# Kernel optimization log

Measured on AMD Instinct MI355X. Metric: run time of the kernel, lower is better.

Reference implementation:

```python
import jax, jax.numpy as jnp
import numpy as np
from math import pi

H = 1024        # hidden_size
CAP = 32        # capacity (even -> CAP//2 even+odd rotation pairs)
EH = H // 2         # even_hidden_size = 512
OH = (H - 1) // 2   # odd_hidden_size  = 511
PAIRS = CAP // 2    # 16

# fixed permutations (hidden_size even branch of the original module)
_PE = np.arange(H).reshape(-1, 2)[:, ::-1].reshape(-1)                       # swap (0,1),(2,3),...
_inner = np.arange(1, 2 * OH + 1).reshape(-1, 2)[:, ::-1].reshape(-1)
_PO = np.concatenate([[0], _inner, [2 * OH + 1]])                            # fix ends, swap interior pairs


def cm(x, y):
    """complex multiply; real/imag stacked in last dim."""
    xr, xi = x[..., 0], x[..., 1]
    yr, yi = y[..., 0], y[..., 1]
    return jnp.stack([xr * yr - xi * yi, xr * yi + xi * yr], -1)


def _ilv(a, b):
    """interleave two [n] vectors -> [2n]."""
    return jnp.stack([a, b], 1).reshape(-1)


def setup_inputs() -> dict:
    key = jax.random.key(0)
    ks = jax.random.split(key, 6)
    u = lambda k, shape: jax.random.uniform(k, shape, jnp.float32) * (2 * pi) - pi
    return {
        "x": jax.random.normal(ks[0], (4096, H, 2), jnp.float32),
        "omega": u(ks[1], (H,)),
        "even_theta": u(ks[2], (PAIRS, EH)),
        "odd_theta": u(ks[3], (PAIRS, OH)),
        "even_phi": u(ks[4], (PAIRS, EH)),
        "odd_phi": u(ks[5], (PAIRS, OH)),
    }


def reference(x, omega, even_theta, odd_theta, even_phi, odd_phi):
    PE = jnp.asarray(_PE)
    PO = jnp.asarray(_PO)

    def step(xc, p):
        et, ep, ot, op = p
        # ---- even rotation (note: original code swaps cos_phi/sin_phi in the
        # call to _v_diag/_v_off_diag; replicated faithfully here) ----
        ct, st, cp, sp = jnp.cos(et), jnp.sin(et), jnp.cos(ep), jnp.sin(ep)
        z = jnp.zeros_like(ct)
        vd = jnp.stack([_ilv(sp * ct, ct), _ilv(cp * ct, z)], -1)          # [H,2]
        vo = jnp.stack([_ilv(-sp * st, st), _ilv(-cp * st, z)], -1)        # [H,2]
        xc = cm(xc, vd) + cm(xc[:, PE, :], vo)
        # ---- odd rotation (ends padded with identity) ----
        ct, st, cp, sp = jnp.cos(ot), jnp.sin(ot), jnp.cos(op), jnp.sin(op)
        z = jnp.zeros_like(ct)
        one = jnp.ones((1,), xc.dtype)
        zero = jnp.zeros((1,), xc.dtype)
        vd_re = jnp.concatenate([one, _ilv(sp * ct, ct), one])
        vd_im = jnp.concatenate([zero, _ilv(cp * ct, z), zero])
        vo_re = jnp.concatenate([zero, _ilv(-sp * st, st), zero])
        vo_im = jnp.concatenate([zero, _ilv(-cp * st, z), zero])
        xc = cm(xc, jnp.stack([vd_re, vd_im], -1)) + cm(xc[:, PO, :], jnp.stack([vo_re, vo_im], -1))
        return xc, None

    x, _ = jax.lax.scan(step, x, (even_theta, even_phi, odd_theta, odd_phi))
    # final diagonal phase
    x = cm(x, jnp.stack([jnp.cos(omega), jnp.sin(omega)], -1))
    return x
```

## Files before the change

kernel.cpp:

```cpp
#include <hip/hip_runtime.h>
#include <math.h>


typedef float f4 __attribute__((ext_vector_type(4)));
typedef _Float16 h4 __attribute__((ext_vector_type(4)));

#define OMCS_OFF 32768

__global__ __launch_bounds__(256) void eunn_precompute(
    const float* __restrict__ omega, const float* __restrict__ et,
    const float* __restrict__ ot, const float* __restrict__ ep,
    const float* __restrict__ op, float* __restrict__ ws) {
  int tid = blockIdx.x * 256 + threadIdx.x;
  if (tid < 16384) {
    int s = tid >> 10, k = tid & 1023;
    int phase = k >> 9, j = k & 511;
    float ct, st, cp, sp;
    if (phase == 0) {
      sincosf(et[s * 512 + j], &st, &ct);
      sincosf(ep[s * 512 + j], &sp, &cp);
    } else if (j < 511) {
      sincosf(ot[s * 511 + j], &st, &ct);
      sincosf(op[s * 511 + j], &sp, &cp);
    } else {
      ct = 1.f; st = 0.f; cp = 0.f; sp = 1.f;
    }
    ((h4*)ws)[s * 1024 + phase * 512 + (j & 7) * 64 + (j >> 3)] =
        (h4){(_Float16)ct, (_Float16)st, (_Float16)cp, (_Float16)sp};
  } else if (tid < 16896) {
    int m = tid - 16384;
    float s0, c0, s1, c1;
    sincosf(omega[2 * m], &s0, &c0);
    sincosf(omega[2 * m + 1], &s1, &c1);
    ((f4*)(ws + OMCS_OFF))[(m & 7) * 64 + (m >> 3)] = (f4){c0, s0, c1, s1};
  }
}

__global__ __launch_bounds__(256, 4) void eunn_main(
    const float* __restrict__ x, float* __restrict__ out,
    const float* __restrict__ ws) {
  const int lane = threadIdx.x & 63;
  const int wid = blockIdx.x * 4 + (threadIdx.x >> 6);
  const h4* cf = (const h4*)ws + lane;

  f4 e[8];
  {
    const f4* xr = (const f4*)(x + (size_t)wid * 2048) + lane * 8;
#pragma unroll
    for (int p = 0; p < 8; ++p) e[p] = xr[p];
  }

  h4 E[8];
#pragma unroll
  for (int p = 0; p < 8; ++p) E[p] = cf[p * 64];

#pragma unroll 1
  for (int s = 0; s < 16; ++s) {
    h4 O[8];
    {
      const h4* ob = cf + s * 1024 + 512;
#pragma unroll
      for (int p = 0; p < 8; ++p) O[p] = ob[p * 64];
    }
#pragma unroll
    for (int p = 0; p < 8; ++p) {
      h4 c = E[p];
      float cx = (float)c.x, cy = (float)c.y, cz = (float)c.z, cw = (float)c.w;
      f4 v = e[p];
      float t0 = cx * v.x - cy * v.z;
      float t1 = cx * v.y - cy * v.w;
      e[p] = (f4){cw * t0 - cz * t1, cz * t0 + cw * t1,
                  cy * v.x + cx * v.z, cy * v.y + cx * v.w};
    }
    {
      const h4* nb = cf + ((s + 1) & 15) * 1024;
#pragma unroll
      for (int p = 0; p < 8; ++p) E[p] = nb[p * 64];
    }
    {
      float ctm = __shfl_up((float)O[7].x, 1, 64);
      float stm = __shfl_up((float)O[7].y, 1, 64);
      if (lane == 0) { ctm = 1.f; stm = 0.f; }
      float upx = __shfl_down(e[0].x, 1, 64);
      float upy = __shfl_down(e[0].y, 1, 64);
      float dnz = __shfl_up(e[7].z, 1, 64);
      float dnw = __shfl_up(e[7].w, 1, 64);
      float nx = stm * dnz + ctm * e[0].x;
      float ny = stm * dnw + ctm * e[0].y;
      e[0].x = nx;
      e[0].y = ny;
#pragma unroll
      for (int p = 0; p < 7; ++p) {
        h4 c = O[p];
        float cx = (float)c.x, cy = (float)c.y, cz = (float)c.z, cw = (float)c.w;
        float e0r = e[p].z, e0i = e[p].w;
        float e1r = e[p + 1].x, e1i = e[p + 1].y;
        float t0 = cx * e0r - cy * e1r;
        float t1 = cx * e0i - cy * e1i;
        e[p].z = cw * t0 - cz * t1;
        e[p].w = cz * t0 + cw * t1;
        e[p + 1].x = cy * e0r + cx * e1r;
        e[p + 1].y = cy * e0i + cx * e1i;
      }
      {
        h4 c = O[7];
        float cx = (float)c.x, cy = (float)c.y, cz = (float)c.z, cw = (float)c.w;
        float e0r = e[7].z, e0i = e[7].w;
        float t0 = cx * e0r - cy * upx;
        float t1 = cx * e0i - cy * upy;
        e[7].z = cw * t0 - cz * t1;
        e[7].w = cz * t0 + cw * t1;
      }
    }
  }

  const f4* om4 = (const f4*)(ws + OMCS_OFF) + lane;
  {
    f4* outr = (f4*)(out + (size_t)wid * 2048) + lane * 8;
#pragma unroll
    for (int p = 0; p < 8; ++p) {
      f4 v = e[p];
      f4 w = om4[p * 64];
      outr[p] = (f4){v.x * w.x - v.y * w.y, v.x * w.y + v.y * w.x,
                     v.z * w.z - v.w * w.w, v.z * w.w + v.w * w.z};
    }
  }
}

extern "C" void kernel_launch(void* const* d_in, const int* in_sizes, int n_in,
                              void* d_out, int out_size, void* d_ws, size_t ws_size,
                              hipStream_t stream) {
  const float* x     = (const float*)d_in[0];
  const float* omega = (const float*)d_in[1];
  const float* et    = (const float*)d_in[2];
  const float* ot    = (const float*)d_in[3];
  const float* ep    = (const float*)d_in[4];
  const float* op    = (const float*)d_in[5];
  float* out = (float*)d_out;
  float* ws  = (float*)d_ws;

  eunn_precompute<<<dim3(66), dim3(256), 0, stream>>>(omega, et, ot, ep, op, ws);

  eunn_main<<<dim3(1024), dim3(256), 0, stream>>>(x, out, ws);
}
```

Before: 134.5 us.

## Stage rotation coefficients in LDS via async global-to-LDS loads

The main kernel now uses 512-thread blocks, each serving 8 rows. It copies the fp16 rotation coefficient table into a 64KB shared-memory buffer in two halves using global_load_lds, with barriers between the halves. Each step then reads its coefficients from LDS instead of issuing per-wave global loads. The aim is less repeated global/L2 traffic and latency for the coefficients. In exchange, 64KB of LDS per block limits occupancy, and the mid-loop reload with barriers stalls every wave in the block.

Result: no change. 133.5 us (-0.7%).

```diff
diff --git a/kernel.cpp b/kernel.cpp
--- a/kernel.cpp
+++ b/kernel.cpp
@@ -36,12 +36,25 @@
   }
 }
 
-__global__ __launch_bounds__(256, 4) void eunn_main(
+__global__ __launch_bounds__(512, 4) void eunn_main(
     const float* __restrict__ x, float* __restrict__ out,
     const float* __restrict__ ws) {
   const int lane = threadIdx.x & 63;
-  const int wid = blockIdx.x * 4 + (threadIdx.x >> 6);
-  const h4* cf = (const h4*)ws + lane;
+  const int wid = blockIdx.x * 8 + (threadIdx.x >> 6);
+
+  __shared__ __attribute__((aligned(16))) char lds[65536];
+
+  {
+    const char* g = (const char*)ws + threadIdx.x * 16;
+#pragma unroll
+    for (int i = 0; i < 8; ++i) {
+      __builtin_amdgcn_global_load_lds(
+          (const __attribute__((address_space(1))) void*)(g + i * 8192),
+          (__attribute__((address_space(3))) void*)(lds + i * 8192 +
+                                                    threadIdx.x * 16),
+          16, 0, 0);
+    }
+  }
 
   f4 e[8];
   {
@@ -50,66 +63,78 @@
     for (int p = 0; p < 8; ++p) e[p] = xr[p];
   }
 
-  h4 E[8];
-#pragma unroll
-  for (int p = 0; p < 8; ++p) E[p] = cf[p * 64];
+  __syncthreads();
 
 #pragma unroll 1
-  for (int s = 0; s < 16; ++s) {
-    h4 O[8];
-    {
-      const h4* ob = cf + s * 1024 + 512;
+  for (int half = 0; half < 2; ++half) {
+    if (half == 1) {
+      __syncthreads();
+      const char* g = (const char*)ws + 65536 + threadIdx.x * 16;
 #pragma unroll
-      for (int p = 0; p < 8; ++p) O[p] = ob[p * 64];
+      for (int i = 0; i < 8; ++i) {
+        __builtin_amdgcn_global_load_lds(
+            (const __attribute__((address_space(1))) void*)(g + i * 8192),
+            (__attribute__((address_space(3))) void*)(lds + i * 8192 +
+                                                      threadIdx.x * 16),
+            16, 0, 0);
+      }
+      __syncthreads();
     }
+#pragma unroll 1
+    for (int s = 0; s < 8; ++s) {
+      const h4* L = (const h4*)lds + s * 1024 + lane;
+      h4 E[8], O[8];
 #pragma unroll
-    for (int p = 0; p < 8; ++p) {
-      h4 c = E[p];
-      float cx = (float)c.x, cy = (float)c.y, cz = (float)c.z, cw = (float)c.w;
-      f4 v = e[p];
-      float t0 = cx * v.x - cy * v.z;
-      float t1 = cx * v.y - cy * v.w;
-      e[p] = (f4){cw * t0 - cz * t1, cz * t0 + cw * t1,
-                  cy * v.x + cx * v.z, cy * v.y + cx * v.w};
-    }
-    {
-      const h4* nb = cf + ((s + 1) & 15) * 1024;
+      for (int p = 0; p < 8; ++p) E[p] = L[p * 64];
 #pragma unroll
-      for (int p = 0; p < 8; ++p) E[p] = nb[p * 64];
-    }
-    {
-      float ctm = __shfl_up((float)O[7].x, 1, 64);
-      float stm = __shfl_up((float)O[7].y, 1, 64);
-      if (lane == 0) { ctm = 1.f; stm = 0.f; }
-      float upx = __shfl_down(e[0].x, 1, 64);
-      float upy = __shfl_down(e[0].y, 1, 64);
-      float dnz = __shfl_up(e[7].z, 1, 64);
-      float dnw = __shfl_up(e[7].w, 1, 64);
-      float nx = stm * dnz + ctm * e[0].x;
-      float ny = stm * dnw + ctm * e[0].y;
-      e[0].x = nx;
-      e[0].y = ny;
+      for (int p = 0; p < 8; ++p) O[p] = L[512 + p * 64];
 #pragma unroll
-      for (int p = 0; p < 7; ++p) {
-        h4 c = O[p];
-        float cx = (float)c.x, cy = (float)c.y, cz = (float)c.z, cw = (float)c.w;
-        float e0r = e[p].z, e0i = e[p].w;
-        float e1r = e[p + 1].x, e1i = e[p + 1].y;
-        float t0 = cx * e0r - cy * e1r;
-        float t1 = cx * e0i - cy * e1i;
-        e[p].z = cw * t0 - cz * t1;
-        e[p].w = cz * t0 + cw * t1;
-        e[p + 1].x = cy * e0r + cx * e1r;
-        e[p + 1].y = cy * e0i + cx * e1i;
+      for (int p = 0; p < 8; ++p) {
+        h4 c = E[p];
+        float cx = (float)c.x, cy = (float)c.y, cz = (float)c.z,
+              cw = (float)c.w;
+        f4 v = e[p];
+        float t0 = cx * v.x - cy * v.z;
+        float t1 = cx * v.y - cy * v.w;
+        e[p] = (f4){cw * t0 - cz * t1, cz * t0 + cw * t1,
+                    cy * v.x + cx * v.z, cy * v.y + cx * v.w};
       }
       {
-        h4 c = O[7];
-        float cx = (float)c.x, cy = (float)c.y, cz = (float)c.z, cw = (float)c.w;
-        float e0r = e[7].z, e0i = e[7].w;
-        float t0 = cx * e0r - cy * upx;
-        float t1 = cx * e0i - cy * upy;
-        e[7].z = cw * t0 - cz * t1;
-        e[7].w = cz * t0 + cw * t1;
+        float ctm = __shfl_up((float)O[7].x, 1, 64);
+        float stm = __shfl_up((float)O[7].y, 1, 64);
+        if (lane == 0) { ctm = 1.f; stm = 0.f; }
+        float upx = __shfl_down(e[0].x, 1, 64);
+        float upy = __shfl_down(e[0].y, 1, 64);
+        float dnz = __shfl_up(e[7].z, 1, 64);
+        float dnw = __shfl_up(e[7].w, 1, 64);
+        float nx = stm * dnz + ctm * e[0].x;
+        float ny = stm * dnw + ctm * e[0].y;
+        e[0].x = nx;
+        e[0].y = ny;
+#pragma unroll
+        for (int p = 0; p < 7; ++p) {
+          h4 c = O[p];
+          float cx = (float)c.x, cy = (float)c.y, cz = (float)c.z,
+                cw = (float)c.w;
+          float e0r = e[p].z, e0i = e[p].w;
+          float e1r = e[p + 1].x, e1i = e[p + 1].y;
+          float t0 = cx * e0r - cy * e1r;
+          float t1 = cx * e0i - cy * e1i;
+          e[p].z = cw * t0 - cz * t1;
+          e[p].w = cz * t0 + cw * t1;
+          e[p + 1].x = cy * e0r + cx * e1r;
+          e[p + 1].y = cy * e0i + cx * e1i;
+        }
+        {
+          h4 c = O[7];
+          float cx = (float)c.x, cy = (float)c.y, cz = (float)c.z,
+                cw = (float)c.w;
+          float e0r = e[7].z, e0i = e[7].w;
+          float t0 = cx * e0r - cy * upx;
+          float t1 = cx * e0i - cy * upy;
+          e[7].z = cw * t0 - cz * t1;
+          e[7].w = cz * t0 + cw * t1;
+        }
       }
     }
   }
@@ -141,5 +166,5 @@
 
   eunn_precompute<<<dim3(66), dim3(256), 0, stream>>>(omega, et, ot, ep, op, ws);
 
-  eunn_main<<<dim3(1024), dim3(256), 0, stream>>>(x, out, ws);
+  eunn_main<<<dim3(512), dim3(512), 0, stream>>>(x, out, ws);
 }
```
